# Kernel tuning notes

Hardware: AMD Instinct MI355X
Metric: run time of the kernel (lower is better)

Reference implementation:

```python
import jax, jax.numpy as jnp
import numpy as np


def setup_inputs() -> dict:
    key = jax.random.key(0)
    inputs = jax.random.normal(key, (4, 1024, 64), dtype=jnp.float32)
    return {"inputs": inputs}


def reference(inputs):
    # inputs: (B, N, D)
    # scores[b,i,j] = sum_d tanh(x[b,i,d] + x[b,j,d])
    addition = inputs[:, :, None, :] + inputs[:, None, :, :]  # (B, N, N, D)
    e_values = jnp.tanh(addition).sum(axis=-1)                # (B, N, N)
    weights = jax.nn.softmax(e_values, axis=-1)               # (B, N, N)
    out = jnp.einsum("bij,bjd->bid", weights, inputs)         # (B, N, D)
    return out
```

## Files before the change

kernel.cpp:

```cpp
#include <hip/hip_runtime.h>


#define NB 4
#define NN 1024
#define ND 64
#define TJ 64
#define TI 8
#define IPW 2
#define NTILES (NN / TJ)

#if __has_builtin(__builtin_amdgcn_exp2f)
#define EXP2F(x) __builtin_amdgcn_exp2f(x)
#else
#define EXP2F(x) exp2f(x)
#endif
#if __has_builtin(__builtin_amdgcn_rcpf)
#define RCPF(x) __builtin_amdgcn_rcpf(x)
#else
#define RCPF(x) (1.0f / (x))
#endif

static constexpr float C_SCALE = 2.8853900817779268f;
static constexpr float K_SHIFT = 46.166241308446828f;

typedef float v2f __attribute__((ext_vector_type(2)));

#define PKFMA(a, b, c) __builtin_elementwise_fma((a), (b), (c))

__device__ __forceinline__ v2f vlo(float4 v) { v2f r; r.x = v.x; r.y = v.y; return r; }
__device__ __forceinline__ v2f vhi(float4 v) { v2f r; r.x = v.z; r.y = v.w; return r; }

__global__ __launch_bounds__(256) void prep_kernel(const float* __restrict__ x,
                                                   float* __restrict__ E) {
    int idx = blockIdx.x * 256 + threadIdx.x;
    float4 v = ((const float4*)x)[idx];
    float4 e;
    e.x = EXP2F(C_SCALE * v.x);
    e.y = EXP2F(C_SCALE * v.y);
    e.z = EXP2F(C_SCALE * v.z);
    e.w = EXP2F(C_SCALE * v.w);
    ((float4*)E)[idx] = e;
}

template <bool HAS_E>
__global__ __launch_bounds__(256) void addattn_kernel(const float* __restrict__ x,
                                                      const float* __restrict__ E,
                                                      float* __restrict__ out) {
    __shared__ float E_lds[TJ * ND];
    __shared__ float x_lds[TJ * ND];
    __shared__ float Ei_lds[TI * ND];
    __shared__ float w_lds[4 * IPW * ND];

    const int tid   = threadIdx.x;
    const int lane  = tid & 63;
    const int wave  = tid >> 6;
    const int wg    = blockIdx.x;
    const int b     = wg >> 7;
    const int ibase = (wg & 127) * TI;

    const float* xb = x + (size_t)b * NN * ND;
    const float* Eb = E + (size_t)b * NN * ND;

    if (tid < TI * ND / 4) {
        if (HAS_E) {
            ((float4*)Ei_lds)[tid] = ((const float4*)(Eb + (size_t)ibase * ND))[tid];
        } else {
            float4 v = ((const float4*)(xb + (size_t)ibase * ND))[tid];
            float4 e;
            e.x = EXP2F(C_SCALE * v.x);
            e.y = EXP2F(C_SCALE * v.y);
            e.z = EXP2F(C_SCALE * v.z);
            e.w = EXP2F(C_SCALE * v.w);
            ((float4*)Ei_lds)[tid] = e;
        }
    }

    v2f acc0a = {0.f, 0.f}, acc0b = {0.f, 0.f};
    v2f acc1a = {0.f, 0.f}, acc1b = {0.f, 0.f};
    float dn0 = 0.f, dn1 = 0.f;

    for (int t = 0; t < NTILES; ++t) {
        __syncthreads();
        {
            const float4* srcx = (const float4*)(xb + (size_t)t * TJ * ND);
            const float4* srcE = (const float4*)(Eb + (size_t)t * TJ * ND);
            #pragma unroll
            for (int it = 0; it < (TJ * ND / 4) / 256; ++it) {
                int idx = it * 256 + tid;
                int j   = idx >> 4;
                int c   = idx & 15;
                float4 xv = srcx[idx];
                ((float4*)x_lds)[idx] = xv;
                float4 ev;
                if (HAS_E) {
                    ev = srcE[idx];
                } else {
                    ev.x = EXP2F(C_SCALE * xv.x);
                    ev.y = EXP2F(C_SCALE * xv.y);
                    ev.z = EXP2F(C_SCALE * xv.z);
                    ev.w = EXP2F(C_SCALE * xv.w);
                }
                *(float4*)&E_lds[j * ND + ((c ^ (j & 15)) << 2)] = ev;
            }
        }
        __syncthreads();

        const int xorkey = lane & 15;
        const float* Ei0 = &Ei_lds[(wave * IPW + 0) * ND];
        const float* Ei1 = &Ei_lds[(wave * IPW + 1) * ND];
        v2f rs0e = {0.f, 0.f}, rs0o = {0.f, 0.f};
        v2f rs1e = {0.f, 0.f}, rs1o = {0.f, 0.f};
        #pragma unroll
        for (int c = 0; c < 16; ++c) {
            float4 ejq = *(const float4*)&E_lds[lane * ND + ((c ^ xorkey) << 2)];
            v2f ej_lo = vlo(ejq), ej_hi = vhi(ejq);
            {
                float4 eiq = *(const float4*)&Ei0[c * 4];
                v2f a = vlo(eiq) * ej_lo;
                v2f q = vhi(eiq) * ej_hi;
                v2f p = a + q;
                v2f r = PKFMA(a, q, p + 1.0f);
                v2f tt; tt.x = RCPF(r.x); tt.y = RCPF(r.y);
                if (c & 1) rs0o = PKFMA(p + 2.0f, tt, rs0o);
                else       rs0e = PKFMA(p + 2.0f, tt, rs0e);
            }
            {
                float4 eiq = *(const float4*)&Ei1[c * 4];
                v2f a = vlo(eiq) * ej_lo;
                v2f q = vhi(eiq) * ej_hi;
                v2f p = a + q;
                v2f r = PKFMA(a, q, p + 1.0f);
                v2f tt; tt.x = RCPF(r.x); tt.y = RCPF(r.y);
                if (c & 1) rs1o = PKFMA(p + 2.0f, tt, rs1o);
                else       rs1e = PKFMA(p + 2.0f, tt, rs1e);
            }
        }
        v2f rs0 = rs0e + rs0o;
        v2f rs1 = rs1e + rs1o;
        float r0 = rs0.x + rs0.y;
        float r1 = rs1.x + rs1.y;
        float w0 = EXP2F(fmaf(-C_SCALE, r0, K_SHIFT));
        float w1 = EXP2F(fmaf(-C_SCALE, r1, K_SHIFT));
        dn0 += w0;
        dn1 += w1;

        w_lds[(wave * IPW + 0) * ND + lane] = w0;
        w_lds[(wave * IPW + 1) * ND + lane] = w1;

        #pragma unroll
        for (int jq = 0; jq < 16; ++jq) {
            float4 w0q = *(const float4*)&w_lds[(wave * IPW + 0) * ND + jq * 4];
            float4 w1q = *(const float4*)&w_lds[(wave * IPW + 1) * ND + jq * 4];
            const int j0 = jq * 4;
            v2f xv01, xv23;
            xv01.x = x_lds[(j0 + 0) * ND + lane];
            xv01.y = x_lds[(j0 + 1) * ND + lane];
            xv23.x = x_lds[(j0 + 2) * ND + lane];
            xv23.y = x_lds[(j0 + 3) * ND + lane];
            acc0a = PKFMA(vlo(w0q), xv01, acc0a);
            acc0b = PKFMA(vhi(w0q), xv23, acc0b);
            acc1a = PKFMA(vlo(w1q), xv01, acc1a);
            acc1b = PKFMA(vhi(w1q), xv23, acc1b);
        }
    }

    #pragma unroll
    for (int s = 0; s < 6; ++s) {
        dn0 += __shfl_xor(dn0, 1 << s, 64);
        dn1 += __shfl_xor(dn1, 1 << s, 64);
    }

    const float num0 = (acc0a.x + acc0a.y) + (acc0b.x + acc0b.y);
    const float num1 = (acc1a.x + acc1a.y) + (acc1b.x + acc1b.y);
    const int i0 = ibase + wave * IPW;
    out[((size_t)b * NN + i0) * ND + lane]     = num0 * RCPF(dn0);
    out[((size_t)b * NN + i0 + 1) * ND + lane] = num1 * RCPF(dn1);
}

extern "C" void kernel_launch(void* const* d_in, const int* in_sizes, int n_in,
                              void* d_out, int out_size, void* d_ws, size_t ws_size,
                              hipStream_t stream) {
    const float* x = (const float*)d_in[0];
    float* out = (float*)d_out;
    const size_t e_bytes = (size_t)NB * NN * ND * sizeof(float);

    dim3 grid(NB * (NN / TI));
    dim3 block(256);

    if (ws_size >= e_bytes) {
        float* E = (float*)d_ws;
        prep_kernel<<<dim3(NB * NN * ND / 4 / 256), dim3(256), 0, stream>>>(x, E);
        addattn_kernel<true><<<grid, block, 0, stream>>>(x, E, out);
    } else {
        addattn_kernel<false><<<grid, block, 0, stream>>>(x, (const float*)nullptr, out);
    }
}
```

Baseline: 78.34 us.

## Keep per-lane output accumulators and reduce via shuffle transpose, drop LDS weight staging

Each lane now owns one key j and accumulates w_ij * x_j across all 64 feature dims in 64 registers per row, reading x from a swizzled LDS layout. This removes the w_lds write/read round trip and the column-strided x reads. A butterfly shuffle-transpose reduction at the end produces the output. The per-row E_i values are read straight from global memory (scalar/uniform loads) instead of LDS. The change raises register pressure, with launch bounds set to 2 blocks, and adds a large cross-lane reduction epilogue.

After: 74.61 us. 1.05x faster.

```diff
diff --git a/kernel.cpp b/kernel.cpp
--- a/kernel.cpp
+++ b/kernel.cpp
@@ -6,7 +6,6 @@
 #define ND 64
 #define TJ 64
 #define TI 8
-#define IPW 2
 #define NTILES (NN / TJ)
 
 #if __has_builtin(__builtin_amdgcn_exp2f)
@@ -43,13 +42,11 @@
 }
 
 template <bool HAS_E>
-__global__ __launch_bounds__(256) void addattn_kernel(const float* __restrict__ x,
-                                                      const float* __restrict__ E,
-                                                      float* __restrict__ out) {
+__global__ __launch_bounds__(256, 2) void addattn_kernel(const float* __restrict__ x,
+                                                         const float* __restrict__ E,
+                                                         float* __restrict__ out) {
     __shared__ float E_lds[TJ * ND];
     __shared__ float x_lds[TJ * ND];
-    __shared__ float Ei_lds[TI * ND];
-    __shared__ float w_lds[4 * IPW * ND];
 
     const int tid   = threadIdx.x;
     const int lane  = tid & 63;
@@ -57,26 +54,20 @@
     const int wg    = blockIdx.x;
     const int b     = wg >> 7;
     const int ibase = (wg & 127) * TI;
-
-    const float* xb = x + (size_t)b * NN * ND;
-    const float* Eb = E + (size_t)b * NN * ND;
-
-    if (tid < TI * ND / 4) {
-        if (HAS_E) {
-            ((float4*)Ei_lds)[tid] = ((const float4*)(Eb + (size_t)ibase * ND))[tid];
-        } else {
-            float4 v = ((const float4*)(xb + (size_t)ibase * ND))[tid];
-            float4 e;
-            e.x = EXP2F(C_SCALE * v.x);
-            e.y = EXP2F(C_SCALE * v.y);
-            e.z = EXP2F(C_SCALE * v.z);
-            e.w = EXP2F(C_SCALE * v.w);
-            ((float4*)Ei_lds)[tid] = e;
-        }
-    }
-
-    v2f acc0a = {0.f, 0.f}, acc0b = {0.f, 0.f};
-    v2f acc1a = {0.f, 0.f}, acc1b = {0.f, 0.f};
+    const int i0    = __builtin_amdgcn_readfirstlane(ibase + wave * 2);
+    const int i1    = i0 + 1;
+
+    const float* xb   = x + (size_t)b * NN * ND;
+    const float* Eb   = E + (size_t)b * NN * ND;
+    const float* Eip0 = Eb + (size_t)i0 * ND;
+    const float* Eip1 = Eb + (size_t)i1 * ND;
+    const float* xip0 = xb + (size_t)i0 * ND;
+    const float* xip1 = xb + (size_t)i1 * ND;
+
+    v2f acc0[32];
+    v2f acc1[32];
+    #pragma unroll
+    for (int k = 0; k < 32; ++k) { acc0[k] = (v2f){0.f, 0.f}; acc1[k] = (v2f){0.f, 0.f}; }
     float dn0 = 0.f, dn1 = 0.f;
 
     for (int t = 0; t < NTILES; ++t) {
@@ -85,12 +76,13 @@
             const float4* srcx = (const float4*)(xb + (size_t)t * TJ * ND);
             const float4* srcE = (const float4*)(Eb + (size_t)t * TJ * ND);
             #pragma unroll
-            for (int it = 0; it < (TJ * ND / 4) / 256; ++it) {
+            for (int it = 0; it < 4; ++it) {
                 int idx = it * 256 + tid;
                 int j   = idx >> 4;
                 int c   = idx & 15;
+                int wof = j * ND + ((c ^ (j & 15)) << 2);
                 float4 xv = srcx[idx];
-                ((float4*)x_lds)[idx] = xv;
+                *(float4*)&x_lds[wof] = xv;
                 float4 ev;
                 if (HAS_E) {
                     ev = srcE[idx];
@@ -100,24 +92,35 @@
                     ev.z = EXP2F(C_SCALE * xv.z);
                     ev.w = EXP2F(C_SCALE * xv.w);
                 }
-                *(float4*)&E_lds[j * ND + ((c ^ (j & 15)) << 2)] = ev;
+                *(float4*)&E_lds[wof] = ev;
             }
         }
         __syncthreads();
 
-        const int xorkey = lane & 15;
-        const float* Ei0 = &Ei_lds[(wave * IPW + 0) * ND];
-        const float* Ei1 = &Ei_lds[(wave * IPW + 1) * ND];
+        const int key = lane & 15;
         v2f rs0e = {0.f, 0.f}, rs0o = {0.f, 0.f};
         v2f rs1e = {0.f, 0.f}, rs1o = {0.f, 0.f};
         #pragma unroll
         for (int c = 0; c < 16; ++c) {
-            float4 ejq = *(const float4*)&E_lds[lane * ND + ((c ^ xorkey) << 2)];
+            float4 ejq = *(const float4*)&E_lds[lane * ND + ((c ^ key) << 2)];
             v2f ej_lo = vlo(ejq), ej_hi = vhi(ejq);
-            {
-                float4 eiq = *(const float4*)&Ei0[c * 4];
-                v2f a = vlo(eiq) * ej_lo;
-                v2f q = vhi(eiq) * ej_hi;
+            v2f e0l, e0h, e1l, e1h;
+            if (HAS_E) {
+                float4 e0q = *(const float4*)&Eip0[c * 4];
+                float4 e1q = *(const float4*)&Eip1[c * 4];
+                e0l = vlo(e0q); e0h = vhi(e0q);
+                e1l = vlo(e1q); e1h = vhi(e1q);
+            } else {
+                float4 x0q = *(const float4*)&xip0[c * 4];
+                float4 x1q = *(const float4*)&xip1[c * 4];
+                e0l.x = EXP2F(C_SCALE * x0q.x); e0l.y = EXP2F(C_SCALE * x0q.y);
+                e0h.x = EXP2F(C_SCALE * x0q.z); e0h.y = EXP2F(C_SCALE * x0q.w);
+                e1l.x = EXP2F(C_SCALE * x1q.x); e1l.y = EXP2F(C_SCALE * x1q.y);
+                e1h.x = EXP2F(C_SCALE * x1q.z); e1h.y = EXP2F(C_SCALE * x1q.w);
+            }
+            {
+                v2f a = e0l * ej_lo;
+                v2f q = e0h * ej_hi;
                 v2f p = a + q;
                 v2f r = PKFMA(a, q, p + 1.0f);
                 v2f tt; tt.x = RCPF(r.x); tt.y = RCPF(r.y);
@@ -125,9 +128,8 @@
                 else       rs0e = PKFMA(p + 2.0f, tt, rs0e);
             }
             {
-                float4 eiq = *(const float4*)&Ei1[c * 4];
-                v2f a = vlo(eiq) * ej_lo;
-                v2f q = vhi(eiq) * ej_hi;
+                v2f a = e1l * ej_lo;
+                v2f q = e1h * ej_hi;
                 v2f p = a + q;
                 v2f r = PKFMA(a, q, p + 1.0f);
                 v2f tt; tt.x = RCPF(r.x); tt.y = RCPF(r.y);
@@ -137,44 +139,54 @@
         }
         v2f rs0 = rs0e + rs0o;
         v2f rs1 = rs1e + rs1o;
-        float r0 = rs0.x + rs0.y;
-        float r1 = rs1.x + rs1.y;
-        float w0 = EXP2F(fmaf(-C_SCALE, r0, K_SHIFT));
-        float w1 = EXP2F(fmaf(-C_SCALE, r1, K_SHIFT));
+        float w0 = EXP2F(fmaf(-C_SCALE, rs0.x + rs0.y, K_SHIFT));
+        float w1 = EXP2F(fmaf(-C_SCALE, rs1.x + rs1.y, K_SHIFT));
         dn0 += w0;
         dn1 += w1;
-
-        w_lds[(wave * IPW + 0) * ND + lane] = w0;
-        w_lds[(wave * IPW + 1) * ND + lane] = w1;
+        v2f w20; w20.x = w0; w20.y = w0;
+        v2f w21; w21.x = w1; w21.y = w1;
 
         #pragma unroll
-        for (int jq = 0; jq < 16; ++jq) {
-            float4 w0q = *(const float4*)&w_lds[(wave * IPW + 0) * ND + jq * 4];
-            float4 w1q = *(const float4*)&w_lds[(wave * IPW + 1) * ND + jq * 4];
-            const int j0 = jq * 4;
-            v2f xv01, xv23;
-            xv01.x = x_lds[(j0 + 0) * ND + lane];
-            xv01.y = x_lds[(j0 + 1) * ND + lane];
-            xv23.x = x_lds[(j0 + 2) * ND + lane];
-            xv23.y = x_lds[(j0 + 3) * ND + lane];
-            acc0a = PKFMA(vlo(w0q), xv01, acc0a);
-            acc0b = PKFMA(vhi(w0q), xv23, acc0b);
-            acc1a = PKFMA(vlo(w1q), xv01, acc1a);
-            acc1b = PKFMA(vhi(w1q), xv23, acc1b);
-        }
-    }
-
+        for (int c = 0; c < 16; ++c) {
+            float4 xq = *(const float4*)&x_lds[lane * ND + ((c ^ key) << 2)];
+            v2f xl = vlo(xq), xh = vhi(xq);
+            acc0[2 * c]     = PKFMA(w20, xl, acc0[2 * c]);
+            acc0[2 * c + 1] = PKFMA(w20, xh, acc0[2 * c + 1]);
+            acc1[2 * c]     = PKFMA(w21, xl, acc1[2 * c]);
+            acc1[2 * c + 1] = PKFMA(w21, xh, acc1[2 * c + 1]);
+        }
+    }
+
+    float* accf0 = (float*)acc0;
+    float* accf1 = (float*)acc1;
+    #pragma unroll
+    for (int s = 0; s < 6; ++s) {
+        const int half = 32 >> s;
+        const int sel  = (lane >> (5 - s)) & 1;
+        #pragma unroll
+        for (int k = 0; k < half; ++k) {
+            {
+                float keep = sel ? accf0[k + half] : accf0[k];
+                float send = sel ? accf0[k] : accf0[k + half];
+                float recv = __shfl_xor(send, half, 64);
+                accf0[k] = keep + recv;
+            }
+            {
+                float keep = sel ? accf1[k + half] : accf1[k];
+                float send = sel ? accf1[k] : accf1[k + half];
+                float recv = __shfl_xor(send, half, 64);
+                accf1[k] = keep + recv;
+            }
+        }
+    }
     #pragma unroll
     for (int s = 0; s < 6; ++s) {
         dn0 += __shfl_xor(dn0, 1 << s, 64);
         dn1 += __shfl_xor(dn1, 1 << s, 64);
     }
 
-    const float num0 = (acc0a.x + acc0a.y) + (acc0b.x + acc0b.y);
-    const float num1 = (acc1a.x + acc1a.y) + (acc1b.x + acc1b.y);
-    const int i0 = ibase + wave * IPW;
-    out[((size_t)b * NN + i0) * ND + lane]     = num0 * RCPF(dn0);
-    out[((size_t)b * NN + i0 + 1) * ND + lane] = num1 * RCPF(dn1);
+    out[((size_t)b * NN + i0) * ND + lane] = accf0[0] * RCPF(dn0);
+    out[((size_t)b * NN + i1) * ND + lane] = accf1[0] * RCPF(dn1);
 }
 
 extern "C" void kernel_launch(void* const* d_in, const int* in_sizes, int n_in,
```
